# Optimization experiments

Measured on AMD Instinct MI355X. Metric: run time of the kernel, lower is better.

The kernel has to match this reference:

```python
import jax, jax.numpy as jnp
import numpy as np
import math

B, L, H, NL, TAG = 32, 64, 200, 2, 6   # dialogues, utterances/dialogue, hidden, GCNII layers, classes
M = 3                                   # modalities (a, v, t)
A = B * L                               # nodes per modality
N = M * A                               # total graph nodes
LAMDA, ALPHA = 0.5, 0.1


def setup_inputs() -> dict:
    key = jax.random.key(0)
    ks = jax.random.split(key, 12)
    s = lambda k, shape: jax.random.normal(k, shape, jnp.float32) * 0.05
    return {
        "x_a": jax.random.normal(ks[0], (B, L, H), jnp.float32),
        "x_v": jax.random.normal(ks[1], (B, L, H), jnp.float32),
        "x_t": jax.random.normal(ks[2], (B, L, H), jnp.float32),
        "fc0_w": s(ks[3], (H, H)),
        "fc0_b": jnp.zeros((H,), jnp.float32),
        "conv_w": s(ks[4], (NL, 2 * H, H)),
        "tm_w": s(ks[5], (M, 2 * H, H)),
        "tm_b": jnp.zeros((M, H), jnp.float32),
        "cross_w": s(ks[6], (6, 3 * H, H)),
        "cross_b": jnp.zeros((6, H), jnp.float32),
        "uni_w": s(ks[7], (M, H, TAG)),
        "uni_b": jnp.zeros((M, TAG), jnp.float32),
    }


def build_adj(feats):
    """feats: [M, A, H]; dialogues are contiguous blocks of L nodes.
    Returns symmetric-normalized [N, N] adjacency (block-diagonal per dialogue
    within each modality, diagonal cross-modal links)."""
    f = feats.reshape(M, B, L, H)
    nrm = f / jnp.linalg.norm(f, axis=-1, keepdims=True)
    # intra-modal per-dialogue cosine-similarity blocks -> angular similarity
    intra = jnp.einsum('mbih,mbjh->mbij', nrm, nrm) * 0.99999
    intra = 1.0 - jnp.arccos(intra) / jnp.pi          # [M,B,L,L]
    # cross-modal per-utterance cosine sim (diagonal entries)
    cross = jnp.einsum('mbih,nbih->mnbi', nrm, nrm) * 0.99999
    cross = 1.0 - jnp.arccos(cross) / jnp.pi          # [M,M,B,L]

    adj = jnp.zeros((N, N), jnp.float32)
    base = jnp.arange(B)[:, None] * L + jnp.arange(L)[None, :]          # [B,L]
    rows = jnp.arange(M)[:, None, None] * A + base[None]                # [M,B,L]
    # intra-modal block-diagonal placement
    adj = adj.at[rows[:, :, :, None], rows[:, :, None, :]].set(intra)
    # cross-modal diagonals (m==n entries equal intra diag, overwrite is identical)
    r = jnp.arange(M)[:, None] * A + jnp.arange(A)[None, :]             # [M,A]
    adj = adj.at[r[:, None, :], r[None, :, :]].set(cross.reshape(M, M, A))
    # symmetric degree normalization D^-1/2 A D^-1/2 (D diagonal -> scale)
    dinv = adj.sum(1) ** -0.5
    return adj * dinv[:, None] * dinv[None, :]


def gcnii(x, adj, fc0_w, fc0_b, conv_w):
    """GCNII (variant=True, use_residue=True). x: [N,H] -> [N,2H]."""
    h = jax.nn.relu(x @ fc0_w + fc0_b)
    h0 = h
    for i in range(NL):
        hi = adj @ h
        support = jnp.concatenate([hi, h0], axis=1)       # variant: [N,2H]
        r = (1.0 - ALPHA) * hi + ALPHA * h0
        beta = math.log(LAMDA / (i + 1) + 1.0)
        h = jax.nn.relu(beta * (support @ conv_w[i]) + (1.0 - beta) * r)
    return jnp.concatenate([x, h], axis=1)                # use_residue


def gated_attention(reps, tm_w, tm_b, cross_w, cross_b):
    """MMGatedAttention. reps: list of M arrays [A, 2H] -> list of M [A, H]."""
    hx = [jax.nn.relu(reps[m] @ tm_w[m] + tm_b[m]) for m in range(M)]
    out, p = [], 0
    for i in range(M):
        hi = jnp.zeros_like(hx[i])
        for j in range(M):
            if i == j:
                continue
            cat = jnp.concatenate([hx[i], hx[j], hx[i] * hx[j]], axis=-1)
            z = jax.nn.sigmoid(cat @ cross_w[p] + cross_b[p])
            hi = hi + z * hx[i] + (1.0 - z) * hx[j]
            p += 1
        out.append(hi)
    return out


def reference(x_a, x_v, x_t, fc0_w, fc0_b, conv_w, tm_w, tm_b,
              cross_w, cross_b, uni_w, uni_b):
    feats = jnp.stack([x_a.reshape(A, H), x_v.reshape(A, H), x_t.reshape(A, H)])  # [M,A,H]
    adj = build_adj(feats)
    big = feats.reshape(N, H)
    g = gcnii(big, adj, fc0_w, fc0_b, conv_w)                 # [N,2H]
    reps = [g[m * A:(m + 1) * A] for m in range(M)]
    h = gated_attention(reps, tm_w, tm_b, cross_w, cross_b)   # M x [A,H]
    logits = [h[m] @ uni_w[m] + uni_b[m] for m in range(M)]
    joint = logits[0] + logits[1] + logits[2]                 # [A, TAG]
    return joint
```

## Files before the change

kernel.cpp:

```cpp
#include <hip/hip_runtime.h>
#include <math.h>

#define H 200
constexpr float INV_PI = 0.31830988618379067f;

typedef __attribute__((ext_vector_type(8))) short bf16x8;
typedef __attribute__((ext_vector_type(4))) float f32x4;
typedef __attribute__((ext_vector_type(4))) short s16x4;

__device__ __forceinline__ short f2bf(float f) {
  unsigned u = __float_as_uint(f);
  u += 0x7FFF + ((u >> 16) & 1);
  return (short)(u >> 16);
}
__device__ __forceinline__ float bf2f(short s) {
  return __uint_as_float(((unsigned)(unsigned short)s) << 16);
}
__device__ __forceinline__ float wave_reduce_sum(float v) {
  #pragma unroll
  for (int off = 32; off; off >>= 1) v += __shfl_down(v, off, 64);
  return v;
}
__device__ __forceinline__ const float* sel_mod(int m, const float* xa, const float* xv,
                                                const float* xt) {
  return (m == 0) ? xa : ((m == 1) ? xv : xt);
}

template <int NK>
__device__ __forceinline__ void gemm_dir(const short* __restrict__ A, int lda,
                                         const short* __restrict__ B, int ldb,
                                         f32x4 acc[4]) {
  const int l = threadIdx.x & 63;
  const int fr = l & 15, fk = (l >> 4) * 8;
  const short* ap = A + fr * lda + fk;
  const short* bp = B + fr * ldb + fk;
  const int ldb16 = 16 * ldb, ldb32 = 32 * ldb, ldb48 = 48 * ldb;
  #pragma unroll
  for (int t = 0; t < NK; t++) {
    bf16x8 a  = *(const bf16x8*)(ap);
    bf16x8 b0 = *(const bf16x8*)(bp);
    bf16x8 b1 = *(const bf16x8*)(bp + ldb16);
    bf16x8 b2 = *(const bf16x8*)(bp + ldb32);
    bf16x8 b3 = *(const bf16x8*)(bp + ldb48);
    acc[0] = __builtin_amdgcn_mfma_f32_16x16x32_bf16(a, b0, acc[0], 0, 0, 0);
    acc[1] = __builtin_amdgcn_mfma_f32_16x16x32_bf16(a, b1, acc[1], 0, 0, 0);
    acc[2] = __builtin_amdgcn_mfma_f32_16x16x32_bf16(a, b2, acc[2], 0, 0, 0);
    acc[3] = __builtin_amdgcn_mfma_f32_16x16x32_bf16(a, b3, acc[3], 0, 0, 0);
    ap += 32; bp += 32;
  }
}

__global__ __launch_bounds__(256) void pack_w_k(
    const float* __restrict__ fc0_w, const float* __restrict__ conv_w,
    const float* __restrict__ tm_w, const float* __restrict__ cross_w,
    short* __restrict__ fc0_wt, short* __restrict__ conv_wt,
    short* __restrict__ tm_wt, short* __restrict__ cross_wt) {
  const int S0 = 208 * 224, S1 = 208 * 416, S2 = 208 * 608;
  const int total = S0 + 5 * S1 + 6 * S2;
  for (int idx = blockIdx.x * 256 + threadIdx.x; idx < total; idx += gridDim.x * 256) {
    const float* src; short* dst; int K, KP, rem;
    if (idx < S0) { src = fc0_w; dst = fc0_wt; K = 200; KP = 224; rem = idx; }
    else if (idx < S0 + 2 * S1) {
      rem = idx - S0; int b = rem / S1; rem -= b * S1;
      src = conv_w + b * 400 * 200; dst = conv_wt + b * S1; K = 400; KP = 416;
    } else if (idx < S0 + 5 * S1) {
      rem = idx - S0 - 2 * S1; int b = rem / S1; rem -= b * S1;
      src = tm_w + b * 400 * 200; dst = tm_wt + b * S1; K = 400; KP = 416;
    } else {
      rem = idx - S0 - 5 * S1; int b = rem / S2; rem -= b * S2;
      src = cross_w + b * 600 * 200; dst = cross_wt + b * S2; K = 600; KP = 608;
    }
    int c = rem / KP, k = rem - c * KP;
    float v = (k < K && c < 200) ? src[k * 200 + c] : 0.f;
    dst[c * KP + k] = f2bf(v);
  }
}

__global__ __launch_bounds__(256) void pack_x_k(
    const float* __restrict__ xa, const float* __restrict__ xv, const float* __restrict__ xt,
    short* __restrict__ bigA, short* __restrict__ tmA, short* __restrict__ convA,
    short* __restrict__ crossA) {
  int tid0 = blockIdx.x * 256 + threadIdx.x, stride = gridDim.x * 256;
  for (int idx = tid0; idx < 6144 * 224; idx += stride) {
    int node = idx / 224, k = idx - node * 224;
    float v = 0.f;
    if (k < 200) { int m = node >> 11, a = node & 2047; v = sel_mod(m, xa, xv, xt)[a * H + k]; }
    short s = f2bf(v);
    bigA[idx] = s;
    if (k < 200) tmA[node * 416 + k] = s;
  }
  for (int idx = tid0; idx < 6144 * 16; idx += stride) {
    int node = idx >> 4, i = idx & 15;
    tmA[node * 416 + 400 + i] = 0;
    convA[node * 416 + 400 + i] = 0;
  }
  for (int idx = tid0; idx < 12288 * 8; idx += stride) {
    int row = idx >> 3, i = idx & 7;
    crossA[row * 608 + 600 + i] = 0;
  }
}

__global__ __launch_bounds__(256) void norms_k(const float* __restrict__ xa,
    const float* __restrict__ xv, const float* __restrict__ xt, float* __restrict__ inv_norm) {
  int u = (blockIdx.x * blockDim.x + threadIdx.x) >> 6;
  int lane = threadIdx.x & 63;
  if (u >= 6144) return;
  int m = u >> 11, a = u & 2047;
  const float* p = sel_mod(m, xa, xv, xt) + a * H;
  float s = 0.f;
  for (int c = lane; c < H; c += 64) { float v = p[c]; s += v * v; }
  s = wave_reduce_sum(s);
  if (lane == 0) inv_norm[u] = 1.f / sqrtf(s);
}

__global__ __launch_bounds__(256) void crossw_k(const float* __restrict__ xa,
    const float* __restrict__ xv, const float* __restrict__ xt,
    const float* __restrict__ inv_norm, float* __restrict__ cw) {
  int g = (blockIdx.x * blockDim.x + threadIdx.x) >> 6;
  int lane = threadIdx.x & 63;
  if (g >= 3 * 2048) return;
  int pair = g >> 11, a = g & 2047;
  int m = (pair == 2) ? 1 : 0;
  int n = (pair == 0) ? 1 : 2;
  const float* pm = sel_mod(m, xa, xv, xt) + a * H;
  const float* pn = sel_mod(n, xa, xv, xt) + a * H;
  float s = 0.f;
  for (int c = lane; c < H; c += 64) s += pm[c] * pn[c];
  s = wave_reduce_sum(s);
  if (lane == 0) {
    float cv = s * inv_norm[m * 2048 + a] * inv_norm[n * 2048 + a] * 0.99999f;
    cv = fminf(fmaxf(cv, -1.f), 1.f);
    cw[g] = 1.f - acosf(cv) * INV_PI;
  }
}

__global__ __launch_bounds__(256) void dinv_k(const float* __restrict__ intra_w,
    const float* __restrict__ cw, float* __restrict__ dinv) {
  int u = (blockIdx.x * blockDim.x + threadIdx.x) >> 6;
  int lane = threadIdx.x & 63;
  if (u >= 6144) return;
  float v = intra_w[(u >> 6) * 4096 + (u & 63) * 64 + lane];
  v = wave_reduce_sum(v);
  if (lane == 0) {
    int m = u >> 11, a = u & 2047;
    float c1 = (m <= 1) ? cw[a] : cw[2048 + a];
    float c2 = (m == 0) ? cw[2048 + a] : cw[2 * 2048 + a];
    dinv[u] = 1.f / sqrtf(v + c1 + c2);
  }
}

__global__ __launch_bounds__(256) void intra_g_k(const short* __restrict__ bigA,
    const float* __restrict__ inv_norm, float* __restrict__ intra, short* __restrict__ intra_b) {
  int mb = blockIdx.x, w = threadIdx.x >> 6;
  f32x4 acc[4] = {};
  gemm_dir<7>(bigA + (mb * 64 + w * 16) * 224, 224, bigA + mb * 64 * 224, 224, acc);
  const int l = threadIdx.x & 63, fr = l & 15, fq = l >> 4;
  int iL0 = w * 16 + fq * 4;
  #pragma unroll
  for (int j = 0; j < 4; j++) {
    int jn = j * 16 + fr;
    float invj = inv_norm[mb * 64 + jn];
    #pragma unroll
    for (int r = 0; r < 4; r++) {
      int iL = iL0 + r;
      float cv = acc[j][r] * inv_norm[mb * 64 + iL] * invj * 0.99999f;
      cv = fminf(fmaxf(cv, -1.f), 1.f);
      float ang = 1.f - acosf(cv) * INV_PI;
      intra[mb * 4096 + iL * 64 + jn] = ang;
      intra_b[mb * 4096 + iL * 64 + jn] = f2bf(ang);
    }
  }
}

__global__ __launch_bounds__(256) void fc0_g_k(const short* __restrict__ fc0_wt,
    const short* __restrict__ bigA, const float* __restrict__ bias,
    const float* __restrict__ dinv, float* __restrict__ h0, short* __restrict__ hs_t,
    short* __restrict__ convA) {
  int w = threadIdx.x >> 6;
  int c0 = blockIdx.y * 16;
  int n0 = blockIdx.x * 256 + w * 64;
  f32x4 acc[4] = {};
  gemm_dir<7>(fc0_wt + c0 * 224, 224, bigA + n0 * 224, 224, acc);
  const int l = threadIdx.x & 63, fr = l & 15, fq = l >> 4;
  int cb = c0 + fq * 4;
  if (cb >= 200) return;
  #pragma unroll
  for (int j = 0; j < 4; j++) {
    int node = n0 + j * 16 + fr;
    float dv = dinv[node];
    f32x4 o; s16x4 ob;
    #pragma unroll
    for (int r = 0; r < 4; r++) {
      float v = fmaxf(acc[j][r] + bias[cb + r], 0.f);
      o[r] = v; ob[r] = f2bf(v);
      hs_t[(cb + r) * 6144 + node] = f2bf(v * dv);
    }
    *(f32x4*)(h0 + node * H + cb) = o;
    *(s16x4*)(convA + node * 416 + 200 + cb) = ob;
  }
}

__global__ __launch_bounds__(256) void adj_g_k(const short* __restrict__ hs_t,
    const short* __restrict__ intra_b, const float* __restrict__ cw,
    const float* __restrict__ dinv, float* __restrict__ hi, short* __restrict__ convA) {
  int mb = blockIdx.x, w = threadIdx.x >> 6;
  int crow0 = blockIdx.y * 64 + w * 16;
  int nbase = mb * 64;
  f32x4 acc[4] = {};
  gemm_dir<2>(hs_t + crow0 * 6144 + nbase, 6144, intra_b + mb * 4096, 64, acc);
  const int l = threadIdx.x & 63, fr = l & 15, fq = l >> 4;
  int cb = crow0 + fq * 4;
  if (cb >= 200) return;
  int m = mb >> 5;
  int n1, n2, p1, p2;
  if (m == 0)      { n1 = 1; p1 = 0; n2 = 2; p2 = 1; }
  else if (m == 1) { n1 = 0; p1 = 0; n2 = 2; p2 = 2; }
  else             { n1 = 0; p1 = 1; n2 = 1; p2 = 2; }
  #pragma unroll
  for (int j = 0; j < 4; j++) {
    int u = nbase + j * 16 + fr;
    int a = u & 2047;
    float w1 = cw[p1 * 2048 + a], w2 = cw[p2 * 2048 + a];
    float dv = dinv[u];
    int o1 = n1 * 2048 + a, o2 = n2 * 2048 + a;
    f32x4 o; s16x4 ob;
    #pragma unroll
    for (int r = 0; r < 4; r++) {
      int c = cb + r;
      float v = dv * (acc[j][r] + w1 * bf2f(hs_t[c * 6144 + o1]) + w2 * bf2f(hs_t[c * 6144 + o2]));
      o[r] = v; ob[r] = f2bf(v);
    }
    *(f32x4*)(hi + u * H + cb) = o;
    *(s16x4*)(convA + u * 416 + cb) = ob;
  }
}

__global__ __launch_bounds__(256) void conv_g_k(const short* __restrict__ Wt,
    const short* __restrict__ convA, const float* __restrict__ hi, const float* __restrict__ h0,
    const float* __restrict__ dinv, float beta, int writeHs, short* __restrict__ hs_t,
    short* __restrict__ tmA) {
  int w = threadIdx.x >> 6;
  int c0 = blockIdx.y * 16;
  int n0 = blockIdx.x * 256 + w * 64;
  f32x4 acc[4] = {};
  gemm_dir<13>(Wt + c0 * 416, 416, convA + n0 * 416, 416, acc);
  const int l = threadIdx.x & 63, fr = l & 15, fq = l >> 4;
  int cb = c0 + fq * 4;
  if (cb >= 200) return;
  float ombeta = 1.f - beta;
  #pragma unroll
  for (int j = 0; j < 4; j++) {
    int node = n0 + j * 16 + fr;
    f32x4 hiv = *(const f32x4*)(hi + node * H + cb);
    f32x4 h0v = *(const f32x4*)(h0 + node * H + cb);
    float dv = dinv[node];
    #pragma unroll
    for (int r = 0; r < 4; r++) {
      float rr = 0.9f * hiv[r] + 0.1f * h0v[r];
      float v = fmaxf(beta * acc[j][r] + ombeta * rr, 0.f);
      if (writeHs) hs_t[(cb + r) * 6144 + node] = f2bf(v * dv);
      else {
      }
      if (!writeHs) tmA[node * 416 + 200 + cb + r] = f2bf(v);
    }
  }
}

__global__ __launch_bounds__(256) void tm_g_k(const short* __restrict__ tm_wt,
    const short* __restrict__ tmA, const float* __restrict__ tmb, float* __restrict__ hx) {
  int m = blockIdx.z, w = threadIdx.x >> 6;
  int c0 = blockIdx.y * 16;
  int n0 = blockIdx.x * 256 + w * 64;
  f32x4 acc[4] = {};
  gemm_dir<13>(tm_wt + m * (208 * 416) + c0 * 416, 416, tmA + (m * 2048 + n0) * 416, 416, acc);
  const int l = threadIdx.x & 63, fr = l & 15, fq = l >> 4;
  int cb = c0 + fq * 4;
  if (cb >= 200) return;
  #pragma unroll
  for (int j = 0; j < 4; j++) {
    int node = m * 2048 + n0 + j * 16 + fr;
    f32x4 o;
    #pragma unroll
    for (int r = 0; r < 4; r++) o[r] = fmaxf(acc[j][r] + tmb[m * H + cb + r], 0.f);
    *(f32x4*)(hx + node * H + cb) = o;
  }
}

__global__ __launch_bounds__(256) void pack_cross_k(const float* __restrict__ hx,
    short* __restrict__ crossA) {
  const int jm_t[6] = {1, 2, 0, 2, 0, 1};
  for (int idx = blockIdx.x * 256 + threadIdx.x; idx < 6 * 2048 * 50;
       idx += gridDim.x * 256) {
    int p = idx / (2048 * 50);
    int rem = idx - p * (2048 * 50);
    int node = rem / 50, c = (rem - node * 50) * 4;
    int im = p >> 1, jm = jm_t[p];
    f32x4 a = *(const f32x4*)(hx + (im * 2048 + node) * H + c);
    f32x4 b = *(const f32x4*)(hx + (jm * 2048 + node) * H + c);
    short* dst = crossA + (p * 2048 + node) * 608;
    s16x4 sa, sb, sp;
    #pragma unroll
    for (int r = 0; r < 4; r++) { sa[r] = f2bf(a[r]); sb[r] = f2bf(b[r]); sp[r] = f2bf(a[r] * b[r]); }
    *(s16x4*)(dst + c) = sa;
    *(s16x4*)(dst + 200 + c) = sb;
    *(s16x4*)(dst + 400 + c) = sp;
  }
}

__global__ __launch_bounds__(256) void crossg_g_k(const short* __restrict__ cross_wt,
    const short* __restrict__ crossA, const float* __restrict__ cb_,
    const float* __restrict__ hx, float* __restrict__ part) {
  const int jm_t[6] = {1, 2, 0, 2, 0, 1};
  int p = blockIdx.z, w = threadIdx.x >> 6;
  int c0 = blockIdx.y * 16;
  int n0 = blockIdx.x * 256 + w * 64;
  f32x4 acc[4] = {};
  gemm_dir<19>(cross_wt + p * (208 * 608) + c0 * 608, 608,
               crossA + (p * 2048 + n0) * 608, 608, acc);
  const int l = threadIdx.x & 63, fr = l & 15, fq = l >> 4;
  int cb = c0 + fq * 4;
  if (cb >= 200) return;
  int im = p >> 1, jm = jm_t[p];
  #pragma unroll
  for (int j = 0; j < 4; j++) {
    int node = n0 + j * 16 + fr;
    f32x4 av = *(const f32x4*)(hx + (im * 2048 + node) * H + cb);
    f32x4 bv = *(const f32x4*)(hx + (jm * 2048 + node) * H + cb);
    f32x4 o;
    #pragma unroll
    for (int r = 0; r < 4; r++) {
      float x = acc[j][r] + cb_[p * H + cb + r];
      float z = 1.f / (1.f + expf(-x));
      o[r] = z * av[r] + (1.f - z) * bv[r];
    }
    *(f32x4*)(part + (p * 2048 + node) * H + cb) = o;
  }
}

__global__ __launch_bounds__(256) void final_k(const float* __restrict__ part,
    const float* __restrict__ uniw, const float* __restrict__ unib, float* __restrict__ out) {
  int a = (blockIdx.x * blockDim.x + threadIdx.x) >> 6;
  int lane = threadIdx.x & 63;
  if (a >= 2048) return;
  float acc[6] = {};
  #pragma unroll
  for (int m = 0; m < 3; m++) {
    const float* pa = part + (2 * m) * 2048 * H + a * H;
    const float* pb = part + (2 * m + 1) * 2048 * H + a * H;
    const float* Wm = uniw + m * H * 6;
    for (int c = lane; c < H; c += 64) {
      float v = pa[c] + pb[c];
      #pragma unroll
      for (int t = 0; t < 6; t++) acc[t] += v * Wm[c * 6 + t];
    }
  }
  #pragma unroll
  for (int t = 0; t < 6; t++) {
    #pragma unroll
    for (int off = 32; off; off >>= 1) acc[t] += __shfl_down(acc[t], off, 64);
  }
  if (lane == 0) {
    #pragma unroll
    for (int t = 0; t < 6; t++)
      out[a * 6 + t] = acc[t] + unib[t] + unib[6 + t] + unib[12 + t];
  }
}

extern "C" void kernel_launch(void* const* d_in, const int* in_sizes, int n_in,
                              void* d_out, int out_size, void* d_ws, size_t ws_size,
                              hipStream_t stream) {
  const float* xa = (const float*)d_in[0];
  const float* xv = (const float*)d_in[1];
  const float* xt = (const float*)d_in[2];
  const float* fc0_w = (const float*)d_in[3];
  const float* fc0_b = (const float*)d_in[4];
  const float* conv_w = (const float*)d_in[5];
  const float* tm_w = (const float*)d_in[6];
  const float* tm_b = (const float*)d_in[7];
  const float* cross_w = (const float*)d_in[8];
  const float* cross_b = (const float*)d_in[9];
  const float* uni_w = (const float*)d_in[10];
  const float* uni_b = (const float*)d_in[11];
  float* out = (float*)d_out;
  float* ws = (float*)d_ws;

  float* inv_norm = ws;
  float* dinv = ws + 6144;
  float* cw = ws + 12288;
  float* intra = ws + 18432;
  float* h0 = ws + 411648;
  float* hi = ws + 1640448;
  float* hx = ws + 2869248;
  float* part = ws + 4098048;
  short* bigA = (short*)(ws + 4098048);
  short* convA = (short*)(ws + 4786176);
  short* tmA = (short*)(ws + 6064128);
  short* crossA = (short*)(ws + 7342080);
  short* hs_t = (short*)(ws + 11077632);
  short* intra_b = (short*)(ws + 11864064);
  short* fc0_wt = (short*)(ws + 12060672);
  short* conv_wt = (short*)(ws + 12083968);
  short* tm_wt = (short*)(ws + 12170496);
  short* cross_wt = (short*)(ws + 12300288);

  pack_w_k<<<2048, 256, 0, stream>>>(fc0_w, conv_w, tm_w, cross_w,
                                     fc0_wt, conv_wt, tm_wt, cross_wt);
  pack_x_k<<<1024, 256, 0, stream>>>(xa, xv, xt, bigA, tmA, convA, crossA);
  norms_k<<<1536, 256, 0, stream>>>(xa, xv, xt, inv_norm);
  crossw_k<<<1536, 256, 0, stream>>>(xa, xv, xt, inv_norm, cw);
  intra_g_k<<<96, 256, 0, stream>>>(bigA, inv_norm, intra, intra_b);
  dinv_k<<<1536, 256, 0, stream>>>(intra, cw, dinv);
  fc0_g_k<<<dim3(24, 13), 256, 0, stream>>>(fc0_wt, bigA, fc0_b, dinv, h0, hs_t, convA);
  adj_g_k<<<dim3(96, 4), 256, 0, stream>>>(hs_t, intra_b, cw, dinv, hi, convA);
  conv_g_k<<<dim3(24, 13), 256, 0, stream>>>(conv_wt, convA, hi, h0, dinv,
                                             0.40546510810816444f, 1, hs_t, tmA);
  adj_g_k<<<dim3(96, 4), 256, 0, stream>>>(hs_t, intra_b, cw, dinv, hi, convA);
  conv_g_k<<<dim3(24, 13), 256, 0, stream>>>(conv_wt + 208 * 416, convA, hi, h0, dinv,
                                             0.22314355131420976f, 0, hs_t, tmA);
  tm_g_k<<<dim3(8, 13, 3), 256, 0, stream>>>(tm_wt, tmA, tm_b, hx);
  pack_cross_k<<<2048, 256, 0, stream>>>(hx, crossA);
  crossg_g_k<<<dim3(8, 13, 6), 256, 0, stream>>>(cross_wt, crossA, cross_b, hx, part);
  final_k<<<512, 256, 0, stream>>>(part, uni_w, uni_b, out);
}
```

Baseline: 204.1 us.

## Fuse preprocessing and epilogue kernels, shrink GEMM tiles, drop fp32 intermediates

```diff
diff --git a/kernel.cpp b/kernel.cpp
--- a/kernel.cpp
+++ b/kernel.cpp
@@ -16,10 +16,9 @@
 __device__ __forceinline__ float bf2f(short s) {
   return __uint_as_float(((unsigned)(unsigned short)s) << 16);
 }
-__device__ __forceinline__ float wave_reduce_sum(float v) {
-  #pragma unroll
-  for (int off = 32; off; off >>= 1) v += __shfl_down(v, off, 64);
-  return v;
+__device__ __forceinline__ float angsim(float c) {
+  c = fminf(fmaxf(c * 0.99999f, -1.f), 1.f);
+  return 1.f - acosf(c) * INV_PI;
 }
 __device__ __forceinline__ const float* sel_mod(int m, const float* xa, const float* xv,
                                                 const float* xt) {
@@ -27,342 +26,319 @@
 }
 
 template <int NK>
-__device__ __forceinline__ void gemm_dir(const short* __restrict__ A, int lda,
-                                         const short* __restrict__ B, int ldb,
-                                         f32x4 acc[4]) {
-  const int l = threadIdx.x & 63;
-  const int fr = l & 15, fk = (l >> 4) * 8;
-  const short* ap = A + fr * lda + fk;
-  const short* bp = B + fr * ldb + fk;
-  const int ldb16 = 16 * ldb, ldb32 = 32 * ldb, ldb48 = 48 * ldb;
+__device__ __forceinline__ void gemm1(const short* __restrict__ A, int lda,
+                                      const short* __restrict__ B, int ldb, f32x4& acc) {
+  const int l = threadIdx.x & 63;
+  const short* ap = A + (l & 15) * lda + (l >> 4) * 8;
+  const short* bp = B + (l & 15) * ldb + (l >> 4) * 8;
   #pragma unroll
   for (int t = 0; t < NK; t++) {
-    bf16x8 a  = *(const bf16x8*)(ap);
-    bf16x8 b0 = *(const bf16x8*)(bp);
-    bf16x8 b1 = *(const bf16x8*)(bp + ldb16);
-    bf16x8 b2 = *(const bf16x8*)(bp + ldb32);
-    bf16x8 b3 = *(const bf16x8*)(bp + ldb48);
+    bf16x8 a = *(const bf16x8*)(ap + t * 32);
+    bf16x8 b = *(const bf16x8*)(bp + t * 32);
+    acc = __builtin_amdgcn_mfma_f32_16x16x32_bf16(a, b, acc, 0, 0, 0);
+  }
+}
+
+template <int NK>
+__device__ __forceinline__ void gemm4(const short* __restrict__ A, int lda,
+                                      const short* __restrict__ B, int ldb, f32x4 acc[4]) {
+  const int l = threadIdx.x & 63;
+  const short* ap = A + (l & 15) * lda + (l >> 4) * 8;
+  const short* bp = B + (l & 15) * ldb + (l >> 4) * 8;
+  const int o16 = 16 * ldb, o32 = 32 * ldb, o48 = 48 * ldb;
+  #pragma unroll
+  for (int t = 0; t < NK; t++) {
+    bf16x8 a = *(const bf16x8*)(ap + t * 32);
+    bf16x8 b0 = *(const bf16x8*)(bp + t * 32);
+    bf16x8 b1 = *(const bf16x8*)(bp + o16 + t * 32);
+    bf16x8 b2 = *(const bf16x8*)(bp + o32 + t * 32);
+    bf16x8 b3 = *(const bf16x8*)(bp + o48 + t * 32);
     acc[0] = __builtin_amdgcn_mfma_f32_16x16x32_bf16(a, b0, acc[0], 0, 0, 0);
     acc[1] = __builtin_amdgcn_mfma_f32_16x16x32_bf16(a, b1, acc[1], 0, 0, 0);
     acc[2] = __builtin_amdgcn_mfma_f32_16x16x32_bf16(a, b2, acc[2], 0, 0, 0);
     acc[3] = __builtin_amdgcn_mfma_f32_16x16x32_bf16(a, b3, acc[3], 0, 0, 0);
-    ap += 32; bp += 32;
-  }
-}
-
-__global__ __launch_bounds__(256) void pack_w_k(
+  }
+}
+
+__global__ __launch_bounds__(256) void pre_k(
+    const float* __restrict__ xa, const float* __restrict__ xv, const float* __restrict__ xt,
     const float* __restrict__ fc0_w, const float* __restrict__ conv_w,
     const float* __restrict__ tm_w, const float* __restrict__ cross_w,
-    short* __restrict__ fc0_wt, short* __restrict__ conv_wt,
-    short* __restrict__ tm_wt, short* __restrict__ cross_wt) {
-  const int S0 = 208 * 224, S1 = 208 * 416, S2 = 208 * 608;
-  const int total = S0 + 5 * S1 + 6 * S2;
-  for (int idx = blockIdx.x * 256 + threadIdx.x; idx < total; idx += gridDim.x * 256) {
-    const float* src; short* dst; int K, KP, rem;
-    if (idx < S0) { src = fc0_w; dst = fc0_wt; K = 200; KP = 224; rem = idx; }
-    else if (idx < S0 + 2 * S1) {
-      rem = idx - S0; int b = rem / S1; rem -= b * S1;
-      src = conv_w + b * 400 * 200; dst = conv_wt + b * S1; K = 400; KP = 416;
+    short* __restrict__ fc0_wt, short* __restrict__ conv_wt, short* __restrict__ tm_wt,
+    short* __restrict__ cross_wt, short* __restrict__ bigA, short* __restrict__ tmA,
+    short* __restrict__ convA, short* __restrict__ hxb,
+    float* __restrict__ inv_norm, float* __restrict__ cw) {
+  const int lane = threadIdx.x & 63;
+  const int wid = blockIdx.x * 4 + (threadIdx.x >> 6);
+
+  if (wid < 6144) {
+    int u = wid, m = u >> 11, a = u & 2047;
+    const float* p = sel_mod(m, xa, xv, xt) + a * H;
+    float v0 = p[lane], v1 = p[lane + 64], v2 = p[lane + 128];
+    float v3 = (lane < 8) ? p[lane + 192] : 0.f;
+    float s = v0 * v0 + v1 * v1 + v2 * v2 + v3 * v3;
+    #pragma unroll
+    for (int off = 32; off; off >>= 1) s += __shfl_down(s, off, 64);
+    if (lane == 0) inv_norm[u] = 1.f / sqrtf(s);
+    short b0 = f2bf(v0), b1 = f2bf(v1), b2 = f2bf(v2), b3 = f2bf(v3);
+    short* br = bigA + u * 224;
+    br[lane] = b0; br[lane + 64] = b1; br[lane + 128] = b2;
+    if (lane < 32) br[192 + lane] = (lane < 8) ? b3 : (short)0;
+    short* tr = tmA + u * 416;
+    tr[lane] = b0; tr[lane + 64] = b1; tr[lane + 128] = b2;
+    if (lane < 8) tr[192 + lane] = b3;
+    if (lane < 16) { tr[400 + lane] = 0; convA[u * 416 + 400 + lane] = 0; }
+    if (lane < 24) hxb[u * 224 + 200 + lane] = 0;
+  } else if (wid < 8192) {
+    int a = wid - 6144;
+    const float* pa = xa + a * H;
+    const float* pv = xv + a * H;
+    const float* pt = xt + a * H;
+    float a0 = pa[lane], a1 = pa[lane + 64], a2 = pa[lane + 128],
+          a3 = (lane < 8) ? pa[lane + 192] : 0.f;
+    float q0 = pv[lane], q1 = pv[lane + 64], q2 = pv[lane + 128],
+          q3 = (lane < 8) ? pv[lane + 192] : 0.f;
+    float t0 = pt[lane], t1 = pt[lane + 64], t2 = pt[lane + 128],
+          t3 = (lane < 8) ? pt[lane + 192] : 0.f;
+    float red[6];
+    red[0] = a0 * a0 + a1 * a1 + a2 * a2 + a3 * a3;
+    red[1] = q0 * q0 + q1 * q1 + q2 * q2 + q3 * q3;
+    red[2] = t0 * t0 + t1 * t1 + t2 * t2 + t3 * t3;
+    red[3] = a0 * q0 + a1 * q1 + a2 * q2 + a3 * q3;
+    red[4] = a0 * t0 + a1 * t1 + a2 * t2 + a3 * t3;
+    red[5] = q0 * t0 + q1 * t1 + q2 * t2 + q3 * t3;
+    #pragma unroll
+    for (int off = 32; off; off >>= 1)
+      #pragma unroll
+      for (int q = 0; q < 6; q++) red[q] += __shfl_down(red[q], off, 64);
+    if (lane == 0) {
+      float ia = 1.f / sqrtf(red[0]), iv = 1.f / sqrtf(red[1]), it = 1.f / sqrtf(red[2]);
+      cw[a] = angsim(red[3] * ia * iv);
+      cw[2048 + a] = angsim(red[4] * ia * it);
+      cw[4096 + a] = angsim(red[5] * iv * it);
+    }
+  }
+
+  const int S0 = 208 * 224, S1 = 208 * 416, S2 = 3 * 208 * 224;
+  const int totalW = S0 + 5 * S1 + 6 * S2;
+  for (int idx = blockIdx.x * 256 + threadIdx.x; idx < totalW; idx += gridDim.x * 256) {
+    if (idx < S0) {
+      int c = idx / 224, k = idx - c * 224;
+      fc0_wt[idx] = (k < 200 && c < 200) ? f2bf(fc0_w[k * 200 + c]) : (short)0;
     } else if (idx < S0 + 5 * S1) {
-      rem = idx - S0 - 2 * S1; int b = rem / S1; rem -= b * S1;
-      src = tm_w + b * 400 * 200; dst = tm_wt + b * S1; K = 400; KP = 416;
+      int rem = idx - S0;
+      int b = rem / S1; rem -= b * S1;
+      int c = rem / 416, k = rem - c * 416;
+      const float* src; short* dst;
+      if (b < 2) { src = conv_w + b * 80000; dst = conv_wt + b * S1; }
+      else { src = tm_w + (b - 2) * 80000; dst = tm_wt + (b - 2) * S1; }
+      dst[c * 416 + k] = (k < 400 && c < 200) ? f2bf(src[k * 200 + c]) : (short)0;
     } else {
-      rem = idx - S0 - 5 * S1; int b = rem / S2; rem -= b * S2;
-      src = cross_w + b * 600 * 200; dst = cross_wt + b * S2; K = 600; KP = 608;
-    }
-    int c = rem / KP, k = rem - c * KP;
-    float v = (k < K && c < 200) ? src[k * 200 + c] : 0.f;
-    dst[c * KP + k] = f2bf(v);
-  }
-}
-
-__global__ __launch_bounds__(256) void pack_x_k(
-    const float* __restrict__ xa, const float* __restrict__ xv, const float* __restrict__ xt,
-    short* __restrict__ bigA, short* __restrict__ tmA, short* __restrict__ convA,
-    short* __restrict__ crossA) {
-  int tid0 = blockIdx.x * 256 + threadIdx.x, stride = gridDim.x * 256;
-  for (int idx = tid0; idx < 6144 * 224; idx += stride) {
-    int node = idx / 224, k = idx - node * 224;
-    float v = 0.f;
-    if (k < 200) { int m = node >> 11, a = node & 2047; v = sel_mod(m, xa, xv, xt)[a * H + k]; }
-    short s = f2bf(v);
-    bigA[idx] = s;
-    if (k < 200) tmA[node * 416 + k] = s;
-  }
-  for (int idx = tid0; idx < 6144 * 16; idx += stride) {
-    int node = idx >> 4, i = idx & 15;
-    tmA[node * 416 + 400 + i] = 0;
-    convA[node * 416 + 400 + i] = 0;
-  }
-  for (int idx = tid0; idx < 12288 * 8; idx += stride) {
-    int row = idx >> 3, i = idx & 7;
-    crossA[row * 608 + 600 + i] = 0;
-  }
-}
-
-__global__ __launch_bounds__(256) void norms_k(const float* __restrict__ xa,
-    const float* __restrict__ xv, const float* __restrict__ xt, float* __restrict__ inv_norm) {
-  int u = (blockIdx.x * blockDim.x + threadIdx.x) >> 6;
-  int lane = threadIdx.x & 63;
-  if (u >= 6144) return;
-  int m = u >> 11, a = u & 2047;
-  const float* p = sel_mod(m, xa, xv, xt) + a * H;
-  float s = 0.f;
-  for (int c = lane; c < H; c += 64) { float v = p[c]; s += v * v; }
-  s = wave_reduce_sum(s);
-  if (lane == 0) inv_norm[u] = 1.f / sqrtf(s);
-}
-
-__global__ __launch_bounds__(256) void crossw_k(const float* __restrict__ xa,
-    const float* __restrict__ xv, const float* __restrict__ xt,
-    const float* __restrict__ inv_norm, float* __restrict__ cw) {
-  int g = (blockIdx.x * blockDim.x + threadIdx.x) >> 6;
-  int lane = threadIdx.x & 63;
-  if (g >= 3 * 2048) return;
-  int pair = g >> 11, a = g & 2047;
-  int m = (pair == 2) ? 1 : 0;
-  int n = (pair == 0) ? 1 : 2;
-  const float* pm = sel_mod(m, xa, xv, xt) + a * H;
-  const float* pn = sel_mod(n, xa, xv, xt) + a * H;
-  float s = 0.f;
-  for (int c = lane; c < H; c += 64) s += pm[c] * pn[c];
-  s = wave_reduce_sum(s);
-  if (lane == 0) {
-    float cv = s * inv_norm[m * 2048 + a] * inv_norm[n * 2048 + a] * 0.99999f;
-    cv = fminf(fmaxf(cv, -1.f), 1.f);
-    cw[g] = 1.f - acosf(cv) * INV_PI;
-  }
-}
-
-__global__ __launch_bounds__(256) void dinv_k(const float* __restrict__ intra_w,
-    const float* __restrict__ cw, float* __restrict__ dinv) {
-  int u = (blockIdx.x * blockDim.x + threadIdx.x) >> 6;
-  int lane = threadIdx.x & 63;
-  if (u >= 6144) return;
-  float v = intra_w[(u >> 6) * 4096 + (u & 63) * 64 + lane];
-  v = wave_reduce_sum(v);
-  if (lane == 0) {
-    int m = u >> 11, a = u & 2047;
-    float c1 = (m <= 1) ? cw[a] : cw[2048 + a];
-    float c2 = (m == 0) ? cw[2048 + a] : cw[2 * 2048 + a];
-    dinv[u] = 1.f / sqrtf(v + c1 + c2);
+      int rem = idx - S0 - 5 * S1;
+      int p = rem / S2; rem -= p * S2;
+      int ph = rem / (208 * 224); rem -= ph * (208 * 224);
+      int c = rem / 224, k = rem - c * 224;
+      cross_wt[((p * 3 + ph) * 208 + c) * 224 + k] =
+          (k < 200 && c < 200) ? f2bf(cross_w[p * 120000 + (ph * 200 + k) * 200 + c]) : (short)0;
+    }
   }
 }
 
 __global__ __launch_bounds__(256) void intra_g_k(const short* __restrict__ bigA,
-    const float* __restrict__ inv_norm, float* __restrict__ intra, short* __restrict__ intra_b) {
-  int mb = blockIdx.x, w = threadIdx.x >> 6;
+    const float* __restrict__ inv_norm, const float* __restrict__ cw,
+    short* __restrict__ intra_b, float* __restrict__ dinv) {
+  const int mb = blockIdx.x, w = threadIdx.x >> 6;
   f32x4 acc[4] = {};
-  gemm_dir<7>(bigA + (mb * 64 + w * 16) * 224, 224, bigA + mb * 64 * 224, 224, acc);
+  gemm4<7>(bigA + (mb * 64 + w * 16) * 224, 224, bigA + mb * 64 * 224, 224, acc);
   const int l = threadIdx.x & 63, fr = l & 15, fq = l >> 4;
-  int iL0 = w * 16 + fq * 4;
+  const int iL0 = w * 16 + fq * 4, u0 = mb * 64;
+  float rsum[4] = {0.f, 0.f, 0.f, 0.f};
   #pragma unroll
   for (int j = 0; j < 4; j++) {
     int jn = j * 16 + fr;
-    float invj = inv_norm[mb * 64 + jn];
-    #pragma unroll
-    for (int r = 0; r < 4; r++) {
-      int iL = iL0 + r;
-      float cv = acc[j][r] * inv_norm[mb * 64 + iL] * invj * 0.99999f;
-      cv = fminf(fmaxf(cv, -1.f), 1.f);
-      float ang = 1.f - acosf(cv) * INV_PI;
-      intra[mb * 4096 + iL * 64 + jn] = ang;
-      intra_b[mb * 4096 + iL * 64 + jn] = f2bf(ang);
+    float invj = inv_norm[u0 + jn];
+    #pragma unroll
+    for (int r = 0; r < 4; r++) {
+      float ang = angsim(acc[j][r] * inv_norm[u0 + iL0 + r] * invj);
+      intra_b[mb * 4096 + (iL0 + r) * 64 + jn] = f2bf(ang);
+      rsum[r] += ang;
+    }
+  }
+  #pragma unroll
+  for (int mask = 1; mask < 16; mask <<= 1)
+    #pragma unroll
+    for (int r = 0; r < 4; r++) rsum[r] += __shfl_xor(rsum[r], mask, 64);
+  if (fr == 0) {
+    int m = u0 >> 11;
+    #pragma unroll
+    for (int r = 0; r < 4; r++) {
+      int u = u0 + iL0 + r, a = u & 2047;
+      float c1 = (m <= 1) ? cw[a] : cw[2048 + a];
+      float c2 = (m == 0) ? cw[2048 + a] : cw[4096 + a];
+      dinv[u] = 1.f / sqrtf(rsum[r] + c1 + c2);
     }
   }
 }
 
 __global__ __launch_bounds__(256) void fc0_g_k(const short* __restrict__ fc0_wt,
     const short* __restrict__ bigA, const float* __restrict__ bias,
-    const float* __restrict__ dinv, float* __restrict__ h0, short* __restrict__ hs_t,
-    short* __restrict__ convA) {
-  int w = threadIdx.x >> 6;
-  int c0 = blockIdx.y * 16;
-  int n0 = blockIdx.x * 256 + w * 64;
-  f32x4 acc[4] = {};
-  gemm_dir<7>(fc0_wt + c0 * 224, 224, bigA + n0 * 224, 224, acc);
-  const int l = threadIdx.x & 63, fr = l & 15, fq = l >> 4;
-  int cb = c0 + fq * 4;
+    const float* __restrict__ dinv, short* __restrict__ convA, short* __restrict__ hs_t) {
+  const int w = threadIdx.x >> 6;
+  const int c0 = blockIdx.y * 16;
+  const int n0 = (blockIdx.x * 4 + w) * 16;
+  f32x4 acc = {};
+  gemm1<7>(fc0_wt + c0 * 224, 224, bigA + n0 * 224, 224, acc);
+  const int l = threadIdx.x & 63;
+  const int node = n0 + (l & 15), cb = c0 + (l >> 4) * 4;
   if (cb >= 200) return;
-  #pragma unroll
-  for (int j = 0; j < 4; j++) {
-    int node = n0 + j * 16 + fr;
-    float dv = dinv[node];
-    f32x4 o; s16x4 ob;
-    #pragma unroll
-    for (int r = 0; r < 4; r++) {
-      float v = fmaxf(acc[j][r] + bias[cb + r], 0.f);
-      o[r] = v; ob[r] = f2bf(v);
-      hs_t[(cb + r) * 6144 + node] = f2bf(v * dv);
-    }
-    *(f32x4*)(h0 + node * H + cb) = o;
-    *(s16x4*)(convA + node * 416 + 200 + cb) = ob;
-  }
+  float dv = dinv[node];
+  s16x4 oh;
+  #pragma unroll
+  for (int r = 0; r < 4; r++) {
+    float v = fmaxf(acc[r] + bias[cb + r], 0.f);
+    oh[r] = f2bf(v);
+    hs_t[(cb + r) * 6144 + node] = f2bf(v * dv);
+  }
+  *(s16x4*)(convA + node * 416 + 200 + cb) = oh;
 }
 
 __global__ __launch_bounds__(256) void adj_g_k(const short* __restrict__ hs_t,
     const short* __restrict__ intra_b, const float* __restrict__ cw,
-    const float* __restrict__ dinv, float* __restrict__ hi, short* __restrict__ convA) {
-  int mb = blockIdx.x, w = threadIdx.x >> 6;
-  int crow0 = blockIdx.y * 64 + w * 16;
-  int nbase = mb * 64;
-  f32x4 acc[4] = {};
-  gemm_dir<2>(hs_t + crow0 * 6144 + nbase, 6144, intra_b + mb * 4096, 64, acc);
-  const int l = threadIdx.x & 63, fr = l & 15, fq = l >> 4;
-  int cb = crow0 + fq * 4;
+    const float* __restrict__ dinv, short* __restrict__ convA) {
+  const int mb = blockIdx.x, w = threadIdx.x >> 6;
+  const int c0 = blockIdx.y * 16;
+  const int nbase = mb * 64, ug = w * 16;
+  f32x4 acc = {};
+  gemm1<2>(hs_t + c0 * 6144 + nbase, 6144, intra_b + mb * 4096 + ug * 64, 64, acc);
+  const int l = threadIdx.x & 63;
+  const int u = nbase + ug + (l & 15), cb = c0 + (l >> 4) * 4;
   if (cb >= 200) return;
-  int m = mb >> 5;
+  const int m = u >> 11, a = u & 2047;
   int n1, n2, p1, p2;
   if (m == 0)      { n1 = 1; p1 = 0; n2 = 2; p2 = 1; }
   else if (m == 1) { n1 = 0; p1 = 0; n2 = 2; p2 = 2; }
   else             { n1 = 0; p1 = 1; n2 = 1; p2 = 2; }
-  #pragma unroll
-  for (int j = 0; j < 4; j++) {
-    int u = nbase + j * 16 + fr;
-    int a = u & 2047;
-    float w1 = cw[p1 * 2048 + a], w2 = cw[p2 * 2048 + a];
-    float dv = dinv[u];
-    int o1 = n1 * 2048 + a, o2 = n2 * 2048 + a;
-    f32x4 o; s16x4 ob;
-    #pragma unroll
-    for (int r = 0; r < 4; r++) {
-      int c = cb + r;
-      float v = dv * (acc[j][r] + w1 * bf2f(hs_t[c * 6144 + o1]) + w2 * bf2f(hs_t[c * 6144 + o2]));
-      o[r] = v; ob[r] = f2bf(v);
-    }
-    *(f32x4*)(hi + u * H + cb) = o;
-    *(s16x4*)(convA + u * 416 + cb) = ob;
-  }
+  float w1 = cw[p1 * 2048 + a], w2 = cw[p2 * 2048 + a];
+  float dv = dinv[u];
+  int o1 = n1 * 2048 + a, o2 = n2 * 2048 + a;
+  s16x4 o;
+  #pragma unroll
+  for (int r = 0; r < 4; r++) {
+    int c = cb + r;
+    float v = dv * (acc[r] + w1 * bf2f(hs_t[c * 6144 + o1]) + w2 * bf2f(hs_t[c * 6144 + o2]));
+    o[r] = f2bf(v);
+  }
+  *(s16x4*)(convA + u * 416 + cb) = o;
 }
 
 __global__ __launch_bounds__(256) void conv_g_k(const short* __restrict__ Wt,
-    const short* __restrict__ convA, const float* __restrict__ hi, const float* __restrict__ h0,
-    const float* __restrict__ dinv, float beta, int writeHs, short* __restrict__ hs_t,
-    short* __restrict__ tmA) {
-  int w = threadIdx.x >> 6;
-  int c0 = blockIdx.y * 16;
-  int n0 = blockIdx.x * 256 + w * 64;
-  f32x4 acc[4] = {};
-  gemm_dir<13>(Wt + c0 * 416, 416, convA + n0 * 416, 416, acc);
-  const int l = threadIdx.x & 63, fr = l & 15, fq = l >> 4;
-  int cb = c0 + fq * 4;
+    const short* __restrict__ convA, const float* __restrict__ dinv, float beta,
+    int writeHs, short* __restrict__ hs_t, short* __restrict__ tmA) {
+  const int w = threadIdx.x >> 6;
+  const int c0 = blockIdx.y * 16;
+  const int n0 = (blockIdx.x * 4 + w) * 16;
+  f32x4 acc = {};
+  gemm1<13>(Wt + c0 * 416, 416, convA + n0 * 416, 416, acc);
+  const int l = threadIdx.x & 63;
+  const int node = n0 + (l & 15), cb = c0 + (l >> 4) * 4;
   if (cb >= 200) return;
+  s16x4 hiv = *(const s16x4*)(convA + node * 416 + cb);
+  s16x4 h0v = *(const s16x4*)(convA + node * 416 + 200 + cb);
   float ombeta = 1.f - beta;
-  #pragma unroll
-  for (int j = 0; j < 4; j++) {
-    int node = n0 + j * 16 + fr;
-    f32x4 hiv = *(const f32x4*)(hi + node * H + cb);
-    f32x4 h0v = *(const f32x4*)(h0 + node * H + cb);
+  if (writeHs) {
     float dv = dinv[node];
     #pragma unroll
     for (int r = 0; r < 4; r++) {
-      float rr = 0.9f * hiv[r] + 0.1f * h0v[r];
-      float v = fmaxf(beta * acc[j][r] + ombeta * rr, 0.f);
-      if (writeHs) hs_t[(cb + r) * 6144 + node] = f2bf(v * dv);
-      else {
-      }
-      if (!writeHs) tmA[node * 416 + 200 + cb + r] = f2bf(v);
-    }
+      float rr = 0.9f * bf2f(hiv[r]) + 0.1f * bf2f(h0v[r]);
+      float v = fmaxf(beta * acc[r] + ombeta * rr, 0.f);
+      hs_t[(cb + r) * 6144 + node] = f2bf(v * dv);
+    }
+  } else {
+    s16x4 o;
+    #pragma unroll
+    for (int r = 0; r < 4; r++) {
+      float rr = 0.9f * bf2f(hiv[r]) + 0.1f * bf2f(h0v[r]);
+      float v = fmaxf(beta * acc[r] + ombeta * rr, 0.f);
+      o[r] = f2bf(v);
+    }
+    *(s16x4*)(tmA + node * 416 + 200 + cb) = o;
   }
 }
 
 __global__ __launch_bounds__(256) void tm_g_k(const short* __restrict__ tm_wt,
-    const short* __restrict__ tmA, const float* __restrict__ tmb, float* __restrict__ hx) {
-  int m = blockIdx.z, w = threadIdx.x >> 6;
-  int c0 = blockIdx.y * 16;
-  int n0 = blockIdx.x * 256 + w * 64;
-  f32x4 acc[4] = {};
-  gemm_dir<13>(tm_wt + m * (208 * 416) + c0 * 416, 416, tmA + (m * 2048 + n0) * 416, 416, acc);
-  const int l = threadIdx.x & 63, fr = l & 15, fq = l >> 4;
-  int cb = c0 + fq * 4;
+    const short* __restrict__ tmA, const float* __restrict__ tmb, short* __restrict__ hxb) {
+  const int m = blockIdx.z, w = threadIdx.x >> 6;
+  const int c0 = blockIdx.y * 16;
+  const int n0 = (blockIdx.x * 4 + w) * 16;
+  f32x4 acc = {};
+  gemm1<13>(tm_wt + m * (208 * 416) + c0 * 416, 416, tmA + (m * 2048 + n0) * 416, 416, acc);
+  const int l = threadIdx.x & 63;
+  const int node = n0 + (l & 15), cb = c0 + (l >> 4) * 4;
   if (cb >= 200) return;
-  #pragma unroll
-  for (int j = 0; j < 4; j++) {
-    int node = m * 2048 + n0 + j * 16 + fr;
-    f32x4 o;
-    #pragma unroll
-    for (int r = 0; r < 4; r++) o[r] = fmaxf(acc[j][r] + tmb[m * H + cb + r], 0.f);
-    *(f32x4*)(hx + node * H + cb) = o;
-  }
-}
-
-__global__ __launch_bounds__(256) void pack_cross_k(const float* __restrict__ hx,
-    short* __restrict__ crossA) {
+  s16x4 o;
+  #pragma unroll
+  for (int r = 0; r < 4; r++) o[r] = f2bf(fmaxf(acc[r] + tmb[m * H + cb + r], 0.f));
+  *(s16x4*)(hxb + (m * 2048 + node) * 224 + cb) = o;
+}
+
+__global__ __launch_bounds__(256) void crossg_g_k(const short* __restrict__ cross_wt,
+    const short* __restrict__ hxb, const float* __restrict__ cb_,
+    const float* __restrict__ uniw, const float* __restrict__ unib, float* __restrict__ out) {
   const int jm_t[6] = {1, 2, 0, 2, 0, 1};
-  for (int idx = blockIdx.x * 256 + threadIdx.x; idx < 6 * 2048 * 50;
-       idx += gridDim.x * 256) {
-    int p = idx / (2048 * 50);
-    int rem = idx - p * (2048 * 50);
-    int node = rem / 50, c = (rem - node * 50) * 4;
-    int im = p >> 1, jm = jm_t[p];
-    f32x4 a = *(const f32x4*)(hx + (im * 2048 + node) * H + c);
-    f32x4 b = *(const f32x4*)(hx + (jm * 2048 + node) * H + c);
-    short* dst = crossA + (p * 2048 + node) * 608;
-    s16x4 sa, sb, sp;
-    #pragma unroll
-    for (int r = 0; r < 4; r++) { sa[r] = f2bf(a[r]); sb[r] = f2bf(b[r]); sp[r] = f2bf(a[r] * b[r]); }
-    *(s16x4*)(dst + c) = sa;
-    *(s16x4*)(dst + 200 + c) = sb;
-    *(s16x4*)(dst + 400 + c) = sp;
-  }
-}
-
-__global__ __launch_bounds__(256) void crossg_g_k(const short* __restrict__ cross_wt,
-    const short* __restrict__ crossA, const float* __restrict__ cb_,
-    const float* __restrict__ hx, float* __restrict__ part) {
-  const int jm_t[6] = {1, 2, 0, 2, 0, 1};
-  int p = blockIdx.z, w = threadIdx.x >> 6;
-  int c0 = blockIdx.y * 16;
-  int n0 = blockIdx.x * 256 + w * 64;
-  f32x4 acc[4] = {};
-  gemm_dir<19>(cross_wt + p * (208 * 608) + c0 * 608, 608,
-               crossA + (p * 2048 + n0) * 608, 608, acc);
-  const int l = threadIdx.x & 63, fr = l & 15, fq = l >> 4;
-  int cb = c0 + fq * 4;
-  if (cb >= 200) return;
-  int im = p >> 1, jm = jm_t[p];
-  #pragma unroll
-  for (int j = 0; j < 4; j++) {
-    int node = n0 + j * 16 + fr;
-    f32x4 av = *(const f32x4*)(hx + (im * 2048 + node) * H + cb);
-    f32x4 bv = *(const f32x4*)(hx + (jm * 2048 + node) * H + cb);
-    f32x4 o;
-    #pragma unroll
-    for (int r = 0; r < 4; r++) {
-      float x = acc[j][r] + cb_[p * H + cb + r];
+  const int p = blockIdx.z, w = threadIdx.x >> 6;
+  const int im = p >> 1, jm = jm_t[p];
+  const int c0 = blockIdx.y * 16;
+  const int n0 = (blockIdx.x * 4 + w) * 16;
+  const short* Wp = cross_wt + p * (3 * 208 * 224);
+  const short* Bi = hxb + (im * 2048 + n0) * 224;
+  const short* Bj = hxb + (jm * 2048 + n0) * 224;
+  f32x4 acc = {};
+  gemm1<7>(Wp + c0 * 224, 224, Bi, 224, acc);
+  gemm1<7>(Wp + 208 * 224 + c0 * 224, 224, Bj, 224, acc);
+  {
+    const int l = threadIdx.x & 63;
+    const short* ap = Wp + 2 * 208 * 224 + (c0 + (l & 15)) * 224 + (l >> 4) * 8;
+    const short* bpi = Bi + (l & 15) * 224 + (l >> 4) * 8;
+    const short* bpj = Bj + (l & 15) * 224 + (l >> 4) * 8;
+    #pragma unroll
+    for (int t = 0; t < 7; t++) {
+      bf16x8 a = *(const bf16x8*)(ap + t * 32);
+      bf16x8 bi = *(const bf16x8*)(bpi + t * 32);
+      bf16x8 bj = *(const bf16x8*)(bpj + t * 32);
+      bf16x8 pr;
+      #pragma unroll
+      for (int e = 0; e < 8; e++) pr[e] = f2bf(bf2f(bi[e]) * bf2f(bj[e]));
+      acc = __builtin_amdgcn_mfma_f32_16x16x32_bf16(a, pr, acc, 0, 0, 0);
+    }
+  }
+  const int l = threadIdx.x & 63;
+  const int node = n0 + (l & 15), cb = c0 + (l >> 4) * 4;
+  float pt[6] = {0.f, 0.f, 0.f, 0.f, 0.f, 0.f};
+  if (cb < 200) {
+    s16x4 ai = *(const s16x4*)(hxb + (im * 2048 + node) * 224 + cb);
+    s16x4 aj = *(const s16x4*)(hxb + (jm * 2048 + node) * 224 + cb);
+    const float* Wu = uniw + im * (H * 6);
+    #pragma unroll
+    for (int r = 0; r < 4; r++) {
+      float x = acc[r] + cb_[p * H + cb + r];
       float z = 1.f / (1.f + expf(-x));
-      o[r] = z * av[r] + (1.f - z) * bv[r];
-    }
-    *(f32x4*)(part + (p * 2048 + node) * H + cb) = o;
-  }
-}
-
-__global__ __launch_bounds__(256) void final_k(const float* __restrict__ part,
-    const float* __restrict__ uniw, const float* __restrict__ unib, float* __restrict__ out) {
-  int a = (blockIdx.x * blockDim.x + threadIdx.x) >> 6;
-  int lane = threadIdx.x & 63;
-  if (a >= 2048) return;
-  float acc[6] = {};
-  #pragma unroll
-  for (int m = 0; m < 3; m++) {
-    const float* pa = part + (2 * m) * 2048 * H + a * H;
-    const float* pb = part + (2 * m + 1) * 2048 * H + a * H;
-    const float* Wm = uniw + m * H * 6;
-    for (int c = lane; c < H; c += 64) {
-      float v = pa[c] + pb[c];
+      float o = z * bf2f(ai[r]) + (1.f - z) * bf2f(aj[r]);
       #pragma unroll
-      for (int t = 0; t < 6; t++) acc[t] += v * Wm[c * 6 + t];
+      for (int t = 0; t < 6; t++) pt[t] += o * Wu[(cb + r) * 6 + t];
     }
   }
   #pragma unroll
   for (int t = 0; t < 6; t++) {
-    #pragma unroll
-    for (int off = 32; off; off >>= 1) acc[t] += __shfl_down(acc[t], off, 64);
-  }
-  if (lane == 0) {
-    #pragma unroll
-    for (int t = 0; t < 6; t++)
-      out[a * 6 + t] = acc[t] + unib[t] + unib[6 + t] + unib[12 + t];
+    pt[t] += __shfl_xor(pt[t], 16, 64);
+    pt[t] += __shfl_xor(pt[t], 32, 64);
+  }
+  if ((l >> 4) == 0) {
+    if (p == 0 && blockIdx.y == 0) {
+      #pragma unroll
+      for (int t = 0; t < 6; t++) pt[t] += unib[t] + unib[6 + t] + unib[12 + t];
+    }
+    #pragma unroll
+    for (int t = 0; t < 6; t++) atomicAdd(out + node * 6 + t, pt[t]);
   }
 }
 
@@ -387,38 +363,29 @@
   float* inv_norm = ws;
   float* dinv = ws + 6144;
   float* cw = ws + 12288;
-  float* intra = ws + 18432;
-  float* h0 = ws + 411648;
-  float* hi = ws + 1640448;
-  float* hx = ws + 2869248;
-  float* part = ws + 4098048;
-  short* bigA = (short*)(ws + 4098048);
-  short* convA = (short*)(ws + 4786176);
-  short* tmA = (short*)(ws + 6064128);
-  short* crossA = (short*)(ws + 7342080);
-  short* hs_t = (short*)(ws + 11077632);
-  short* intra_b = (short*)(ws + 11864064);
-  short* fc0_wt = (short*)(ws + 12060672);
-  short* conv_wt = (short*)(ws + 12083968);
-  short* tm_wt = (short*)(ws + 12170496);
-  short* cross_wt = (short*)(ws + 12300288);
-
-  pack_w_k<<<2048, 256, 0, stream>>>(fc0_w, conv_w, tm_w, cross_w,
-                                     fc0_wt, conv_wt, tm_wt, cross_wt);
-  pack_x_k<<<1024, 256, 0, stream>>>(xa, xv, xt, bigA, tmA, convA, crossA);
-  norms_k<<<1536, 256, 0, stream>>>(xa, xv, xt, inv_norm);
-  crossw_k<<<1536, 256, 0, stream>>>(xa, xv, xt, inv_norm, cw);
-  intra_g_k<<<96, 256, 0, stream>>>(bigA, inv_norm, intra, intra_b);
-  dinv_k<<<1536, 256, 0, stream>>>(intra, cw, dinv);
-  fc0_g_k<<<dim3(24, 13), 256, 0, stream>>>(fc0_wt, bigA, fc0_b, dinv, h0, hs_t, convA);
-  adj_g_k<<<dim3(96, 4), 256, 0, stream>>>(hs_t, intra_b, cw, dinv, hi, convA);
-  conv_g_k<<<dim3(24, 13), 256, 0, stream>>>(conv_wt, convA, hi, h0, dinv,
+  short* bigA = (short*)(ws + 18432);
+  short* convA = (short*)(ws + 706560);
+  short* tmA = (short*)(ws + 1984512);
+  short* hxb = (short*)(ws + 3262464);
+  short* hs_t = (short*)(ws + 3950592);
+  short* intra_b = (short*)(ws + 4589568);
+  short* fc0_wt = (short*)(ws + 4786176);
+  short* conv_wt = (short*)(ws + 4809472);
+  short* tm_wt = (short*)(ws + 4896000);
+  short* cross_wt = (short*)(ws + 5025792);
+
+  hipMemsetAsync(out, 0, (size_t)out_size * sizeof(float), stream);
+  pre_k<<<2048, 256, 0, stream>>>(xa, xv, xt, fc0_w, conv_w, tm_w, cross_w,
+                                  fc0_wt, conv_wt, tm_wt, cross_wt,
+                                  bigA, tmA, convA, hxb, inv_norm, cw);
+  intra_g_k<<<96, 256, 0, stream>>>(bigA, inv_norm, cw, intra_b, dinv);
+  fc0_g_k<<<dim3(96, 13), 256, 0, stream>>>(fc0_wt, bigA, fc0_b, dinv, convA, hs_t);
+  adj_g_k<<<dim3(96, 13), 256, 0, stream>>>(hs_t, intra_b, cw, dinv, convA);
+  conv_g_k<<<dim3(96, 13), 256, 0, stream>>>(conv_wt, convA, dinv,
                                              0.40546510810816444f, 1, hs_t, tmA);
-  adj_g_k<<<dim3(96, 4), 256, 0, stream>>>(hs_t, intra_b, cw, dinv, hi, convA);
-  conv_g_k<<<dim3(24, 13), 256, 0, stream>>>(conv_wt + 208 * 416, convA, hi, h0, dinv,
+  adj_g_k<<<dim3(96, 13), 256, 0, stream>>>(hs_t, intra_b, cw, dinv, convA);
+  conv_g_k<<<dim3(96, 13), 256, 0, stream>>>(conv_wt + 208 * 416, convA, dinv,
                                              0.22314355131420976f, 0, hs_t, tmA);
-  tm_g_k<<<dim3(8, 13, 3), 256, 0, stream>>>(tm_wt, tmA, tm_b, hx);
-  pack_cross_k<<<2048, 256, 0, stream>>>(hx, crossA);
-  crossg_g_k<<<dim3(8, 13, 6), 256, 0, stream>>>(cross_wt, crossA, cross_b, hx, part);
-  final_k<<<512, 256, 0, stream>>>(part, uni_w, uni_b, out);
-}
+  tm_g_k<<<dim3(32, 13, 3), 256, 0, stream>>>(tm_wt, tmA, tm_b, hxb);
+  crossg_g_k<<<dim3(32, 13, 6), 256, 0, stream>>>(cross_wt, hxb, cross_b, uni_w, uni_b, out);
+}
```

New measurement: 177.6 us. -13.0%, faster.
